# Kernel optimization log

Hardware: AMD Instinct MI355X
Metric: run time of the kernel (lower is better)

Reference implementation:

```python
import jax, jax.numpy as jnp
import numpy as np

K = 10
EPS = 1e-5  # BatchNorm eps, eval mode with running_mean=0, running_var=1


def mish(x):
    return x * jnp.tanh(jax.nn.softplus(x))


def knn_idx(x, k):
    # x: (B, C, N); returns (B, N, k) indices of k nearest neighbors (incl. self)
    xx = jnp.sum(x * x, axis=1)                      # (B, N)
    inner = jnp.einsum('bcn,bcm->bnm', x, x)         # (B, N, N)
    neg_d = 2.0 * inner - xx[:, :, None] - xx[:, None, :]
    return jax.lax.top_k(neg_d, k)[1]


def graph_feature(x, k):
    # x: (B, C, N) -> edge features (B, 2C, N, k): cat(nbr - x, x)
    idx = knn_idx(x, k)
    x_t = jnp.transpose(x, (0, 2, 1))                # (B, N, C)
    nbr = jax.vmap(lambda xt, ix: xt[ix])(x_t, idx)  # (B, N, k, C)
    ctr = jnp.broadcast_to(x_t[:, :, None, :], nbr.shape)
    edge = jnp.concatenate([nbr - ctr, ctr], axis=-1)
    return jnp.transpose(edge, (0, 3, 1, 2))


def block2d(x, W, g, b):
    # Conv2d(kernel=1, bias=False) + BatchNorm2d(eval) + Mish
    y = jnp.einsum('oi,bink->bonk', W, x)
    y = y * (g / jnp.sqrt(1.0 + EPS))[None, :, None, None] + b[None, :, None, None]
    return mish(y)


def block1d(x, W, g, b):
    # Conv1d(kernel=1, bias=False) + BatchNorm1d(eval) + Mish
    y = jnp.einsum('oi,bin->bon', W, x)
    y = y * (g / jnp.sqrt(1.0 + EPS))[None, :, None] + b[None, :, None]
    return mish(y)


def setup_inputs() -> dict:
    key = jax.random.key(0)
    ks = jax.random.split(key, 32)
    B, N = 8, 4096
    x = jax.random.normal(ks[0], (B, 3, N), dtype=jnp.float32)

    def w(k, o, i):
        return jax.random.normal(k, (o, i), dtype=jnp.float32) * np.float32(np.sqrt(2.0 / i))

    W1 = w(ks[1], 64, 6)
    W2 = w(ks[2], 64, 128)
    W3 = w(ks[3], 128, 128)
    W4 = w(ks[4], 128, 128)
    W5 = w(ks[5], 128, 256)
    W6 = w(ks[6], 64, 128)
    W7 = w(ks[7], 64, 128)
    W8 = w(ks[8], 64, 128)
    W9 = w(ks[9], 2, 64)

    bn_sizes = [64, 64, 128, 128, 128, 64, 64, 64]
    gs, bs = [], []
    for i, c in enumerate(bn_sizes):
        gs.append(1.0 + 0.1 * jax.random.normal(ks[10 + i], (c,), dtype=jnp.float32))
        bs.append(0.1 * jax.random.normal(ks[20 + i], (c,), dtype=jnp.float32))

    d = {'x': x, 'W1': W1, 'W2': W2, 'W3': W3, 'W4': W4, 'W5': W5,
         'W6': W6, 'W7': W7, 'W8': W8, 'W9': W9}
    for i in range(8):
        d['g%d' % (i + 1)] = gs[i]
        d['b%d' % (i + 1)] = bs[i]
    return d


def reference(x, W1, W2, W3, W4, W5, W6, W7, W8, W9,
              g1, g2, g3, g4, g5, g6, g7, g8,
              b1, b2, b3, b4, b5, b6, b7, b8):
    e = graph_feature(x, K)                      # (B, 6, N, k)
    x1 = jnp.max(block2d(e, W1, g1, b1), axis=-1)  # (B, 64, N)
    e = graph_feature(x1, K)                     # (B, 128, N, k)
    x2 = jnp.max(block2d(e, W2, g2, b2), axis=-1)  # (B, 64, N)
    e = graph_feature(x2, K)                     # (B, 128, N, k)
    x3 = jnp.max(block2d(e, W3, g3, b3), axis=-1)  # (B, 128, N)
    h = block1d(x3, W4, g4, b4)                  # (B, 128, N)
    h = block1d(jnp.concatenate([h, x3], axis=1), W5, g5, b5)  # (B, 128, N)
    h = block1d(h, W6, g6, b6)                   # (B, 64, N)
    h = block1d(jnp.concatenate([h, x2], axis=1), W7, g7, b7)  # (B, 64, N)
    h = block1d(jnp.concatenate([h, x1], axis=1), W8, g8, b8)  # (B, 64, N)
    return jnp.einsum('oi,bin->bon', W9, h)      # (B, 2, N)
```

## Files before the change

kernel.cpp:

```cpp
#include <hip/hip_runtime.h>
#include <hip/hip_bf16.h>
#include <math.h>
#include <float.h>

#define B_ 8
#define N_ 4096
#define M_ (B_*N_)
#define KNN 10

typedef unsigned long long ull;
typedef __attribute__((ext_vector_type(8))) short s16x8;
typedef __attribute__((ext_vector_type(4))) float f32x4;

__device__ __forceinline__ float mishf(float x){
  float sp = (x > 20.f) ? x : __logf(1.f + __expf(x));
  float e2 = __expf(-2.f*sp);
  float th = (1.f - e2) / (1.f + e2);
  return x * th;
}

__device__ __forceinline__ ull shfl_xor_u64(ull v, int mask){
  unsigned lo = (unsigned)v, hi = (unsigned)(v >> 32);
  lo = (unsigned)__shfl_xor((int)lo, mask);
  hi = (unsigned)__shfl_xor((int)hi, mask);
  return ((ull)hi << 32) | lo;
}
__device__ __forceinline__ ull shfl_u64(ull v, int src){
  unsigned lo = (unsigned)v, hi = (unsigned)(v >> 32);
  lo = (unsigned)__shfl((int)lo, src);
  hi = (unsigned)__shfl((int)hi, src);
  return ((ull)hi << 32) | lo;
}
__device__ __forceinline__ int mbcnt_lt(ull mask){
  return __builtin_amdgcn_mbcnt_hi((unsigned)(mask>>32),
         __builtin_amdgcn_mbcnt_lo((unsigned)mask, 0));
}
__device__ __forceinline__ unsigned mono_u32(float f){
  unsigned u = __float_as_uint(f);
  return u ^ ((unsigned)((int)u >> 31) | 0x80000000u);
}
__device__ __forceinline__ float unmono(unsigned vk){
  unsigned u = (vk & 0x80000000u) ? (vk ^ 0x80000000u) : ~vk;
  return __uint_as_float(u);
}

__global__ __launch_bounds__(256) void k_transpose_x(const float* __restrict__ x,
                                                     float* __restrict__ xp){
  int n = blockIdx.x*256 + threadIdx.x;
  if (n >= M_) return;
  int b = n >> 12, i = n & (N_-1);
  const float* xb = x + (size_t)b*3*N_;
  float v0 = xb[i], v1 = xb[N_+i], v2 = xb[2*N_+i];
  float* o = xp + (size_t)n*3;
  o[0]=v0; o[1]=v1; o[2]=v2;
}

template<int C>
__global__ __launch_bounds__(256) void k_xx(const float* __restrict__ X,
                                            float* __restrict__ xx){
  int n = blockIdx.x*256 + threadIdx.x;
  if (n >= M_) return;
  const float* r = X + (size_t)n*C;
  float s = 0.f;
#pragma unroll
  for (int c=0;c<C;c++){ float v=r[c]; s = fmaf(v,v,s); }
  xx[n] = s;
}

__global__ __launch_bounds__(256) void k_cvt(const float* __restrict__ X,
                                             ushort* __restrict__ Xhi,
                                             ushort* __restrict__ Xlo){
  int i = blockIdx.x*256 + threadIdx.x;
  const float4* src = (const float4*)X + (size_t)i*2;
  float4 v0 = src[0], v1 = src[1];
  float vv[8] = {v0.x,v0.y,v0.z,v0.w,v1.x,v1.y,v1.z,v1.w};
  ushort h[8], l[8];
#pragma unroll
  for (int e=0;e<8;e++){
    __hip_bfloat16 hb = __float2bfloat16(vv[e]);
    float hf = __bfloat162float(hb);
    __hip_bfloat16 lb = __float2bfloat16(vv[e]-hf);
    h[e] = *(ushort*)&hb; l[e] = *(ushort*)&lb;
  }
  uint4 hp, lp;
  hp.x = (unsigned)h[0] | ((unsigned)h[1]<<16);
  hp.y = (unsigned)h[2] | ((unsigned)h[3]<<16);
  hp.z = (unsigned)h[4] | ((unsigned)h[5]<<16);
  hp.w = (unsigned)h[6] | ((unsigned)h[7]<<16);
  lp.x = (unsigned)l[0] | ((unsigned)l[1]<<16);
  lp.y = (unsigned)l[2] | ((unsigned)l[3]<<16);
  lp.z = (unsigned)l[4] | ((unsigned)l[5]<<16);
  lp.w = (unsigned)l[6] | ((unsigned)l[7]<<16);
  *(uint4*)(Xhi + (size_t)i*8) = hp;
  *(uint4*)(Xlo + (size_t)i*8) = lp;
}

__global__ __launch_bounds__(256,2) void k_knn64m(const ushort* __restrict__ Xhi,
                                                  const ushort* __restrict__ Xlo,
                                                  const float* __restrict__ xx,
                                                  int* __restrict__ idxout){
  constexpr int JT  = 128;
  constexpr int CAP = 320;
  __shared__ ushort XJhi[JT*64];
  __shared__ ushort XJlo[JT*64];
  __shared__ float  halfxx[JT];
  __shared__ ull    buf[4][CAP];

  const int t    = threadIdx.x;
  const int w    = t >> 6;
  const int lane = t & 63;
  const int b    = blockIdx.x & 7;
  const int i0   = (blockIdx.x >> 3) * 64;
  const float* xxb = xx + (size_t)b*N_;

  const int arow = i0 + w*16 + (lane & 15);
  const ushort* Ah = Xhi + ((size_t)(b*N_ + arow))*64;
  const ushort* Al = Xlo + ((size_t)(b*N_ + arow))*64;
  const int ko = (lane >> 4)*8;
  s16x8 aH0 = *(const s16x8*)(Ah + ko);
  s16x8 aH1 = *(const s16x8*)(Ah + 32 + ko);
  s16x8 aL0 = *(const s16x8*)(Al + ko);
  s16x8 aL1 = *(const s16x8*)(Al + 32 + ko);

  ull kq[KNN];
#pragma unroll
  for (int q=0;q<KNN;q++) kq[q]=0ull;
  float Treg = -INFINITY;

  for (int jt = 0; jt < N_/JT; ++jt){
    const int j0 = jt*JT;
    {
      const int r = t & 127;
      const ushort* src = ((t < 128) ? Xhi : Xlo) + ((size_t)(b*N_ + j0 + r))*64;
      char* dst = (char*)((t < 128) ? XJhi : XJlo) + r*128;
      const unsigned sw = ((unsigned)(r & 7)) << 4;
#pragma unroll
      for (int c=0;c<8;c++){
        uint4 v = *(const uint4*)(src + c*8);
        *(uint4*)(dst + ((unsigned)(c*16) ^ sw)) = v;
      }
    }
    if (t < JT) halfxx[t] = 0.5f*xxb[j0+t];
    __syncthreads();

    f32x4 acc[8];
#pragma unroll
    for (int cb=0;cb<8;cb++) acc[cb] = (f32x4){0.f,0.f,0.f,0.f};

#pragma unroll
    for (int cb=0;cb<8;cb++){
      const int brow = cb*16 + (lane & 15);
      const unsigned sw = ((unsigned)(brow & 7)) << 4;
      const char* ph = (const char*)XJhi + brow*128;
      const char* pl = (const char*)XJlo + brow*128;
      const int kb0 = (int)((unsigned)((lane>>4)<<4) ^ sw);
      const int kb1 = (int)((unsigned)(64 | ((lane>>4)<<4)) ^ sw);
      s16x8 bh0 = *(const s16x8*)(ph + kb0);
      s16x8 bl0 = *(const s16x8*)(pl + kb0);
      s16x8 bh1 = *(const s16x8*)(ph + kb1);
      s16x8 bl1 = *(const s16x8*)(pl + kb1);
      f32x4 a = acc[cb];
      a = __builtin_amdgcn_mfma_f32_16x16x32_bf16(aH0, bh0, a, 0,0,0);
      a = __builtin_amdgcn_mfma_f32_16x16x32_bf16(aH0, bl0, a, 0,0,0);
      a = __builtin_amdgcn_mfma_f32_16x16x32_bf16(aL0, bh0, a, 0,0,0);
      a = __builtin_amdgcn_mfma_f32_16x16x32_bf16(aL0, bl0, a, 0,0,0);
      a = __builtin_amdgcn_mfma_f32_16x16x32_bf16(aH1, bh1, a, 0,0,0);
      a = __builtin_amdgcn_mfma_f32_16x16x32_bf16(aH1, bl1, a, 0,0,0);
      a = __builtin_amdgcn_mfma_f32_16x16x32_bf16(aL1, bh1, a, 0,0,0);
      a = __builtin_amdgcn_mfma_f32_16x16x32_bf16(aL1, bl1, a, 0,0,0);
      acc[cb] = a;
    }

    float hx[8];
#pragma unroll
    for (int cb=0;cb<8;cb++) hx[cb] = halfxx[cb*16 + (lane & 15)];

    if (jt == 0){
#pragma unroll
      for (int reg=0;reg<4;reg++){
        const unsigned rl = (unsigned)((lane>>4)*4 + reg);
        ull k8[8];
#pragma unroll
        for (int cb=0;cb<8;cb++){
          float v = acc[cb][reg] - hx[cb];
          unsigned jinv = 4095u - (unsigned)(cb*16 + (lane & 15));
          k8[cb] = ((ull)mono_u32(v)<<32) | ((ull)jinv<<4) | rl;
        }
#pragma unroll
        for (int q=0;q<KNN;q++){
          ull m = k8[0];
#pragma unroll
          for (int s=1;s<8;s++) m = m > k8[s] ? m : k8[s];
          ull v1 = shfl_xor_u64(m,1); m = m>v1?m:v1;
          ull v2 = shfl_xor_u64(m,2); m = m>v2?m:v2;
          ull v4 = shfl_xor_u64(m,4); m = m>v4?m:v4;
          ull v8 = shfl_xor_u64(m,8); m = m>v8?m:v8;
          ull mv = shfl_u64(m, (lane>>2)<<4);
          if (lane < 16 && (lane&3)==reg) kq[q] = mv;
#pragma unroll
          for (int s=0;s<8;s++) k8[s] = (k8[s]==m) ? 0ull : k8[s];
        }
      }
      Treg = unmono((unsigned)(kq[KNN-1] >> 32));
    } else {
      float Tf[4];
#pragma unroll
      for (int reg=0;reg<4;reg++) Tf[reg] = __shfl(Treg, (lane>>4)*4 + reg);
      int cnt = 0;
#pragma unroll
      for (int cb=0;cb<8;cb++){
#pragma unroll
        for (int reg=0;reg<4;reg++){
          float v = acc[cb][reg] - hx[cb];
          bool pass = v >= Tf[reg];
          ull mask = __ballot(pass);
          if (mask){
            if (pass){
              int slot = cnt + mbcnt_lt(mask);
              unsigned jinv = 4095u - (unsigned)(j0 + cb*16 + (lane & 15));
              ull key = ((ull)mono_u32(v)<<32) | ((ull)jinv<<4)
                        | (unsigned)((lane>>4)*4 + reg);
              if (slot < CAP) buf[w][slot] = key;
            }
            cnt += __popcll(mask);
          }
        }
      }
      if (cnt){
        int nb = cnt < CAP ? cnt : CAP;
        for (int e=0;e<nb;e++){
          ull k64 = buf[w][e];
          if ((int)(k64 & 15ull) == lane && k64 > kq[KNN-1]){
            ull ck = k64;
#pragma unroll
            for (int q=0;q<KNN;q++){
              ull hi = ck > kq[q] ? ck : kq[q];
              ull lo = ck > kq[q] ? kq[q] : ck;
              kq[q] = hi; ck = lo;
            }
          }
        }
        Treg = unmono((unsigned)(kq[KNN-1] >> 32));
      }
    }
    __syncthreads();
  }

  if (lane < 16){
    int* o = idxout + ((size_t)b*N_ + i0 + w*16 + lane)*KNN;
#pragma unroll
    for (int q=0;q<KNN;q++) o[q] = (int)(4095u - (unsigned)((kq[q]>>4) & 4095ull));
  }
}

template<int C>
__global__ __launch_bounds__(256,2) void k_knn(const float* __restrict__ X,
                                               const float* __restrict__ xx,
                                               int* __restrict__ idxout){
  constexpr bool BIG = (C % 4 == 0);
  constexpr int LS  = BIG ? (C + 4) : 12;
  constexpr int NC4 = BIG ? (C/4 + 1) : 1;
  constexpr int JT  = 128;
  constexpr int CAP = 320;
  __shared__ float XI[64*LS];
  __shared__ float XJ[JT*LS];
  __shared__ ull   buf[4][CAP];

  const int t    = threadIdx.x;
  const int w    = t >> 6;
  const int lane = t & 63;
  const int b    = blockIdx.y;
  const int i0   = blockIdx.x*64;
  const int tc   = t & 15, tr = t >> 4;
  const float* Xb  = X  + (size_t)b*N_*C;
  const float* xxb = xx + (size_t)b*N_;

  if constexpr (BIG){
    for (int f = t; f < 64*(C/4); f += 256){
      int r = f >> 4, c4 = f & 15;
      *(float4*)&XI[r*LS + c4*4] = *(const float4*)&Xb[(size_t)(i0+r)*C + c4*4];
    }
    if (t < 64){ XI[t*LS+C]=1.f; XI[t*LS+C+1]=0.f; XI[t*LS+C+2]=0.f; XI[t*LS+C+3]=0.f; }
  } else {
    if (t < 64){
      const float* p = &Xb[(size_t)(i0+t)*C];
      XI[t*LS+0]=p[0]; XI[t*LS+1]=p[1]; XI[t*LS+2]=p[2]; XI[t*LS+3]=1.f;
    }
  }

  ull kq[KNN];
#pragma unroll
  for (int q=0;q<KNN;q++) kq[q]=0ull;
  float Treg = -INFINITY;

  for (int jt = 0; jt < N_/JT; ++jt){
    const int j0 = jt*JT;
    if constexpr (BIG){
      for (int f = t; f < JT*(C/4); f += 256){
        int r = f >> 4, c4 = f & 15;
        *(float4*)&XJ[r*LS + c4*4] = *(const float4*)&Xb[(size_t)(j0+r)*C + c4*4];
      }
      if (t < JT){ XJ[t*LS+C] = -0.5f*xxb[j0+t]; XJ[t*LS+C+1]=0.f; XJ[t*LS+C+2]=0.f; XJ[t*LS+C+3]=0.f; }
    } else {
      if (t < JT){
        const float* p = &Xb[(size_t)(j0+t)*C];
        XJ[t*LS+0]=p[0]; XJ[t*LS+1]=p[1]; XJ[t*LS+2]=p[2]; XJ[t*LS+3]=-0.5f*xxb[j0+t];
      }
    }
    __syncthreads();

    float acc[4][8];
#pragma unroll
    for (int rr=0;rr<4;rr++)
#pragma unroll
      for (int s=0;s<8;s++) acc[rr][s]=0.f;

#pragma unroll 2
    for (int c4 = 0; c4 < NC4; ++c4){
      float4 xi0 = *(const float4*)&XI[(tr*4+0)*LS + c4*4];
      float4 xi1 = *(const float4*)&XI[(tr*4+1)*LS + c4*4];
      float4 xi2 = *(const float4*)&XI[(tr*4+2)*LS + c4*4];
      float4 xi3 = *(const float4*)&XI[(tr*4+3)*LS + c4*4];
#pragma unroll
      for (int s=0;s<8;s++){
        float4 xj = *(const float4*)&XJ[(tc+16*s)*LS + c4*4];
        float a0=acc[0][s], a1=acc[1][s], a2=acc[2][s], a3=acc[3][s];
        a0=fmaf(xi0.x,xj.x,a0); a1=fmaf(xi1.x,xj.x,a1); a2=fmaf(xi2.x,xj.x,a2); a3=fmaf(xi3.x,xj.x,a3);
        a0=fmaf(xi0.y,xj.y,a0); a1=fmaf(xi1.y,xj.y,a1); a2=fmaf(xi2.y,xj.y,a2); a3=fmaf(xi3.y,xj.y,a3);
        a0=fmaf(xi0.z,xj.z,a0); a1=fmaf(xi1.z,xj.z,a1); a2=fmaf(xi2.z,xj.z,a2); a3=fmaf(xi3.z,xj.z,a3);
        a0=fmaf(xi0.w,xj.w,a0); a1=fmaf(xi1.w,xj.w,a1); a2=fmaf(xi2.w,xj.w,a2); a3=fmaf(xi3.w,xj.w,a3);
        acc[0][s]=a0; acc[1][s]=a1; acc[2][s]=a2; acc[3][s]=a3;
      }
    }

    if (jt == 0){
#pragma unroll
      for (int rr=0;rr<4;rr++){
        const unsigned rl = (unsigned)((lane>>4)*4 + rr);
        ull k8[8];
#pragma unroll
        for (int s=0;s<8;s++){
          unsigned jinv = 4095u - (unsigned)(tc + 16*s);
          k8[s] = ((ull)mono_u32(acc[rr][s])<<32) | ((ull)jinv<<4) | rl;
        }
#pragma unroll
        for (int q=0;q<KNN;q++){
          ull m = k8[0];
#pragma unroll
          for (int s=1;s<8;s++) m = m > k8[s] ? m : k8[s];
          ull v1 = shfl_xor_u64(m,1); m = m>v1?m:v1;
          ull v2 = shfl_xor_u64(m,2); m = m>v2?m:v2;
          ull v4 = shfl_xor_u64(m,4); m = m>v4?m:v4;
          ull v8 = shfl_xor_u64(m,8); m = m>v8?m:v8;
          ull mv = shfl_u64(m, (lane>>2)<<4);
          if (lane < 16 && (lane&3)==rr) kq[q] = mv;
#pragma unroll
          for (int s=0;s<8;s++) k8[s] = (k8[s]==m) ? 0ull : k8[s];
        }
      }
      Treg = unmono((unsigned)(kq[KNN-1] >> 32));
    } else {
      float Tf[4];
#pragma unroll
      for (int rr=0;rr<4;rr++) Tf[rr] = __shfl(Treg, (lane>>4)*4 + rr);
      int cnt = 0;
#pragma unroll
      for (int s=0;s<8;s++){
#pragma unroll
        for (int rr=0;rr<4;rr++){
          bool pass = acc[rr][s] >= Tf[rr];
          ull mask = __ballot(pass);
          if (mask){
            if (pass){
              int slot = cnt + mbcnt_lt(mask);
              unsigned jinv = 4095u - (unsigned)(j0 + tc + 16*s);
              ull key = ((ull)mono_u32(acc[rr][s])<<32) | ((ull)jinv<<4)
                        | (unsigned)((lane>>4)*4 + rr);
              if (slot < CAP) buf[w][slot] = key;
            }
            cnt += __popcll(mask);
          }
        }
      }
      if (cnt){
        int nb = cnt < CAP ? cnt : CAP;
        for (int e=0;e<nb;e++){
          ull k64 = buf[w][e];
          if ((int)(k64 & 15ull) == lane && k64 > kq[KNN-1]){
            ull ck = k64;
#pragma unroll
            for (int q=0;q<KNN;q++){
              ull hi = ck > kq[q] ? ck : kq[q];
              ull lo = ck > kq[q] ? kq[q] : ck;
              kq[q] = hi; ck = lo;
            }
          }
        }
        Treg = unmono((unsigned)(kq[KNN-1] >> 32));
      }
    }
    __syncthreads();
  }

  if (lane < 16){
    int* o = idxout + ((size_t)b*N_ + i0 + w*16 + lane)*KNN;
#pragma unroll
    for (int q=0;q<KNN;q++) o[q] = (int)(4095u - (unsigned)((kq[q]>>4) & 4095ull));
  }
}

template<int PT>
__global__ __launch_bounds__(256) void k_gemm(
    const float* __restrict__ X1, int C1,
    const float* __restrict__ X2, int C2,
    const float* __restrict__ W, int hmask, int hshift, int wstride, int hoff,
    const float* __restrict__ g, const float* __restrict__ bb, int act,
    float* __restrict__ Y, int Pfull)
{
  constexpr int CPT = PT/16;
  constexpr int WLS = PT + 4;
  __shared__ float Xt[32*68];
  __shared__ float Wt[32*WLS];
  const int t  = threadIdx.x;
  const int r0 = blockIdx.x*64;
  const int p0 = blockIdx.y*PT;
  const int cg = t & 15, rg = t >> 4;
  const int C = C1 + C2;
  const int nkt = (C + 31) >> 5;

  float acc[4][CPT];
#pragma unroll
  for (int a=0;a<4;a++)
#pragma unroll
    for (int c=0;c<CPT;c++) acc[a][c]=0.f;

  for (int kt = 0; kt < nkt; ++kt){
    const int k0 = kt*32;
#pragma unroll
    for (int e = t; e < 64*32; e += 256){
      int kk = e & 31, r = e >> 5;
      int gk = k0 + kk;
      float v = 0.f;
      if (gk < C1) v = X1[(size_t)(r0+r)*C1 + gk];
      else if (gk < C) v = X2[(size_t)(r0+r)*C2 + (gk - C1)];
      Xt[kk*68 + r] = v;
    }
#pragma unroll
    for (int e = t; e < PT*32; e += 256){
      int kk = e & 31, p = e >> 5;
      int gp = p0 + p;
      int wrow = (gp & hmask)*wstride + (gp >> hshift)*hoff;
      int gk = k0 + kk;
      Wt[kk*WLS + p] = (gk < C) ? W[(size_t)wrow + gk] : 0.f;
    }
    __syncthreads();
#pragma unroll
    for (int kk=0;kk<32;kk++){
      float4 xv = *(const float4*)&Xt[kk*68 + rg*4];
      float xr[4] = {xv.x, xv.y, xv.z, xv.w};
      float wv[CPT];
#pragma unroll
      for (int c4=0;c4<CPT/4;c4++){
        float4 w4 = *(const float4*)&Wt[kk*WLS + cg*CPT + c4*4];
        wv[c4*4+0]=w4.x; wv[c4*4+1]=w4.y; wv[c4*4+2]=w4.z; wv[c4*4+3]=w4.w;
      }
#pragma unroll
      for (int rr=0;rr<4;rr++)
#pragma unroll
        for (int cc=0;cc<CPT;cc++)
          acc[rr][cc] = fmaf(xr[rr], wv[cc], acc[rr][cc]);
    }
    __syncthreads();
  }

  const float srs = rsqrtf(1.f + 1e-5f);
  float sv[CPT], bvv[CPT];
#pragma unroll
  for (int cc=0;cc<CPT;cc++){
    int gp = p0 + cg*CPT + cc;
    if (g){ sv[cc] = g[gp]*srs; bvv[cc] = bb[gp]; } else { sv[cc]=1.f; bvv[cc]=0.f; }
  }
#pragma unroll
  for (int rr=0;rr<4;rr++){
    size_t row = r0 + rg*4 + rr;
    float* yr = Y + row*(size_t)Pfull + p0 + cg*CPT;
#pragma unroll
    for (int c4=0;c4<CPT/4;c4++){
      float y0 = sv[c4*4+0]*acc[rr][c4*4+0] + bvv[c4*4+0];
      float y1 = sv[c4*4+1]*acc[rr][c4*4+1] + bvv[c4*4+1];
      float y2 = sv[c4*4+2]*acc[rr][c4*4+2] + bvv[c4*4+2];
      float y3 = sv[c4*4+3]*acc[rr][c4*4+3] + bvv[c4*4+3];
      if (act){ y0=mishf(y0); y1=mishf(y1); y2=mishf(y2); y3=mishf(y3); }
      *(float4*)&yr[c4*4] = make_float4(y0,y1,y2,y3);
    }
  }
}

template<int O>
__global__ __launch_bounds__(256) void k_edgemax(
    const float* __restrict__ ua, const int* __restrict__ idx,
    const float* __restrict__ g, const float* __restrict__ bb,
    float* __restrict__ Y)
{
  constexpr int TPR = O/4;
  const int gt = blockIdx.x*256 + threadIdx.x;
  const int m  = gt / TPR;
  const int og = gt % TPR;
  if (m >= M_) return;
  const int base = m & ~(N_-1);
  const int P = 2*O;
  const float4 u0 = *(const float4*)&ua[(size_t)m*P + og*4];
  const float4 a0 = *(const float4*)&ua[(size_t)m*P + O + og*4];
  const float srs = rsqrtf(1.f + 1e-5f);
  const float4 gv  = *(const float4*)&g[og*4];
  const float4 bv4 = *(const float4*)&bb[og*4];
  const float sx = gv.x*srs, sy = gv.y*srs, sz = gv.z*srs, sw = gv.w*srs;
  const float cx = a0.x - u0.x, cy = a0.y - u0.y, cz = a0.z - u0.z, cw = a0.w - u0.w;
  float mx = -INFINITY, my = -INFINITY, mz = -INFINITY, mw = -INFINITY;
  const int* id = idx + (size_t)m*KNN;
#pragma unroll
  for (int k=0;k<KNN;k++){
    int j = id[k];
    const float4 uj = *(const float4*)&ua[(size_t)(base + j)*P + og*4];
    float zx = fmaf(sx, uj.x + cx, bv4.x);
    float zy = fmaf(sy, uj.y + cy, bv4.y);
    float zz = fmaf(sz, uj.z + cz, bv4.z);
    float zw = fmaf(sw, uj.w + cw, bv4.w);
    mx = fmaxf(mx, mishf(zx));
    my = fmaxf(my, mishf(zy));
    mz = fmaxf(mz, mishf(zz));
    mw = fmaxf(mw, mishf(zw));
  }
  *(float4*)&Y[(size_t)m*O + og*4] = make_float4(mx,my,mz,mw);
}

__global__ __launch_bounds__(256) void k_final(const float* __restrict__ h,
                                               const float* __restrict__ W9,
                                               float* __restrict__ out){
  __shared__ float w[128];
  const int t = threadIdx.x;
  if (t < 128) w[t] = W9[t];
  __syncthreads();
  const int m = blockIdx.x*256 + t;
  if (m >= M_) return;
  const int b = m >> 12, i = m & (N_-1);
  const float* hr = h + (size_t)m*64;
  float s0 = 0.f, s1 = 0.f;
#pragma unroll
  for (int c=0;c<64;c++){ float v = hr[c]; s0 = fmaf(w[c], v, s0); s1 = fmaf(w[64+c], v, s1); }
  out[((size_t)b*2 + 0)*N_ + i] = s0;
  out[((size_t)b*2 + 1)*N_ + i] = s1;
}

extern "C" void kernel_launch(void* const* d_in, const int* in_sizes, int n_in,
                              void* d_out, int out_size, void* d_ws, size_t ws_size,
                              hipStream_t stream)
{
  const float* x  = (const float*)d_in[0];
  const float* W1 = (const float*)d_in[1];
  const float* W2 = (const float*)d_in[2];
  const float* W3 = (const float*)d_in[3];
  const float* W4 = (const float*)d_in[4];
  const float* W5 = (const float*)d_in[5];
  const float* W6 = (const float*)d_in[6];
  const float* W7 = (const float*)d_in[7];
  const float* W8 = (const float*)d_in[8];
  const float* W9 = (const float*)d_in[9];
  const float* g1 = (const float*)d_in[10]; const float* b1 = (const float*)d_in[11];
  const float* g2 = (const float*)d_in[12]; const float* b2 = (const float*)d_in[13];
  const float* g3 = (const float*)d_in[14]; const float* b3 = (const float*)d_in[15];
  const float* g4 = (const float*)d_in[16]; const float* b4 = (const float*)d_in[17];
  const float* g5 = (const float*)d_in[18]; const float* b5 = (const float*)d_in[19];
  const float* g6 = (const float*)d_in[20]; const float* b6 = (const float*)d_in[21];
  const float* g7 = (const float*)d_in[22]; const float* b7 = (const float*)d_in[23];
  const float* g8 = (const float*)d_in[24]; const float* b8 = (const float*)d_in[25];
  float* out = (float*)d_out;

  float* ws  = (float*)d_ws;
  float* xp  = ws;
  float* xx  = xp + 98304;
  int*   idx = (int*)(xx + 32768);
  float* ua  = (float*)(idx + 327680);
  float* x1  = ua + 8388608;
  float* x2  = x1 + 2097152;
  float* x3  = x2 + 2097152;
  float* h4  = x3 + 4194304;
  float* h5  = h4 + 4194304;
  float* h6  = x3;
  float* h7  = h4;
  float* h8  = h5;
  ushort* Xhi = (ushort*)ua;
  ushort* Xlo = (ushort*)(ua + 1048576);

  const dim3 blk(256);
  const float* nullf = nullptr;

  k_transpose_x<<<dim3(M_/256), blk, 0, stream>>>(x, xp);
  k_xx<3><<<dim3(M_/256), blk, 0, stream>>>(xp, xx);
  k_knn<3><<<dim3(N_/64, B_), blk, 0, stream>>>(xp, xx, idx);
  k_gemm<128><<<dim3(M_/64, 1), blk, 0, stream>>>(xp, 3, nullf, 0,
      W1, 63, 6, 6, 3, nullf, nullf, 0, ua, 128);
  k_edgemax<64><<<dim3(M_*16/256), blk, 0, stream>>>(ua, idx, g1, b1, x1);

  k_xx<64><<<dim3(M_/256), blk, 0, stream>>>(x1, xx);
  k_cvt<<<dim3(M_*64/(8*256)), blk, 0, stream>>>(x1, Xhi, Xlo);
  k_knn64m<<<dim3(512), blk, 0, stream>>>(Xhi, Xlo, xx, idx);
  k_gemm<128><<<dim3(M_/64, 1), blk, 0, stream>>>(x1, 64, nullf, 0,
      W2, 63, 6, 128, 64, nullf, nullf, 0, ua, 128);
  k_edgemax<64><<<dim3(M_*16/256), blk, 0, stream>>>(ua, idx, g2, b2, x2);

  k_xx<64><<<dim3(M_/256), blk, 0, stream>>>(x2, xx);
  k_cvt<<<dim3(M_*64/(8*256)), blk, 0, stream>>>(x2, Xhi, Xlo);
  k_knn64m<<<dim3(512), blk, 0, stream>>>(Xhi, Xlo, xx, idx);
  k_gemm<128><<<dim3(M_/64, 2), blk, 0, stream>>>(x2, 64, nullf, 0,
      W3, 127, 7, 128, 64, nullf, nullf, 0, ua, 256);
  k_edgemax<128><<<dim3(M_*32/256), blk, 0, stream>>>(ua, idx, g3, b3, x3);

  k_gemm<128><<<dim3(M_/64, 1), blk, 0, stream>>>(x3, 128, nullf, 0,
      W4, 127, 7, 128, 0, g4, b4, 1, h4, 128);
  k_gemm<128><<<dim3(M_/64, 1), blk, 0, stream>>>(h4, 128, x3, 128,
      W5, 127, 7, 256, 0, g5, b5, 1, h5, 128);
  k_gemm<64><<<dim3(M_/64, 1), blk, 0, stream>>>(h5, 128, nullf, 0,
      W6, 63, 6, 128, 0, g6, b6, 1, h6, 64);
  k_gemm<64><<<dim3(M_/64, 1), blk, 0, stream>>>(h6, 64, x2, 64,
      W7, 63, 6, 128, 0, g7, b7, 1, h7, 64);
  k_gemm<64><<<dim3(M_/64, 1), blk, 0, stream>>>(h7, 64, x1, 64,
      W8, 63, 6, 128, 0, g8, b8, 1, h8, 64);
  k_final<<<dim3(M_/256), blk, 0, stream>>>(h8, W9, out);
}
```

Baseline: 1.647 ms.

## Split KNN candidate range in halves across blocks and merge partial top-k

```diff
diff --git a/kernel.cpp b/kernel.cpp
--- a/kernel.cpp
+++ b/kernel.cpp
@@ -95,11 +95,11 @@
   *(uint4*)(Xlo + (size_t)i*8) = lp;
 }
 
-__global__ __launch_bounds__(256,2) void k_knn64m(const ushort* __restrict__ Xhi,
+__global__ __launch_bounds__(256,4) void k_knn64m(const ushort* __restrict__ Xhi,
                                                   const ushort* __restrict__ Xlo,
                                                   const float* __restrict__ xx,
-                                                  int* __restrict__ idxout){
-  constexpr int JT  = 128;
+                                                  ull* __restrict__ part){
+  constexpr int JT  = 64;
   constexpr int CAP = 320;
   __shared__ ushort XJhi[JT*64];
   __shared__ ushort XJlo[JT*64];
@@ -109,8 +109,12 @@
   const int t    = threadIdx.x;
   const int w    = t >> 6;
   const int lane = t & 63;
-  const int b    = blockIdx.x & 7;
-  const int i0   = (blockIdx.x >> 3) * 64;
+  const int bid  = blockIdx.x;
+  const int b    = bid & 7;
+  const int rest = bid >> 3;
+  const int i0   = (rest >> 1) * 64;
+  const int half = rest & 1;
+  const int jbase = half * 2048;
   const float* xxb = xx + (size_t)b*N_;
 
   const int arow = i0 + w*16 + (lane & 15);
@@ -127,28 +131,30 @@
   for (int q=0;q<KNN;q++) kq[q]=0ull;
   float Treg = -INFINITY;
 
-  for (int jt = 0; jt < N_/JT; ++jt){
-    const int j0 = jt*JT;
+  for (int jt = 0; jt < 2048/JT; ++jt){
+    const int j0g = jbase + jt*JT;
     {
-      const int r = t & 127;
-      const ushort* src = ((t < 128) ? Xhi : Xlo) + ((size_t)(b*N_ + j0 + r))*64;
-      char* dst = (char*)((t < 128) ? XJhi : XJlo) + r*128;
+      const int bsel = t >> 7;
+      const int r    = (t >> 1) & 63;
+      const int cq   = (t & 1) * 4;
+      const ushort* src = (bsel ? Xlo : Xhi) + ((size_t)(b*N_ + j0g + r))*64 + cq*8;
+      char* dst = (char*)(bsel ? XJlo : XJhi) + r*128;
       const unsigned sw = ((unsigned)(r & 7)) << 4;
 #pragma unroll
-      for (int c=0;c<8;c++){
+      for (int c=0;c<4;c++){
         uint4 v = *(const uint4*)(src + c*8);
-        *(uint4*)(dst + ((unsigned)(c*16) ^ sw)) = v;
-      }
-    }
-    if (t < JT) halfxx[t] = 0.5f*xxb[j0+t];
+        *(uint4*)(dst + ((unsigned)((cq+c)*16) ^ sw)) = v;
+      }
+    }
+    if (t < JT) halfxx[t] = 0.5f*xxb[j0g+t];
     __syncthreads();
 
-    f32x4 acc[8];
-#pragma unroll
-    for (int cb=0;cb<8;cb++) acc[cb] = (f32x4){0.f,0.f,0.f,0.f};
-
-#pragma unroll
-    for (int cb=0;cb<8;cb++){
+    f32x4 acc[4];
+#pragma unroll
+    for (int cb=0;cb<4;cb++) acc[cb] = (f32x4){0.f,0.f,0.f,0.f};
+
+#pragma unroll
+    for (int cb=0;cb<4;cb++){
       const int brow = cb*16 + (lane & 15);
       const unsigned sw = ((unsigned)(brow & 7)) << 4;
       const char* ph = (const char*)XJhi + brow*128;
@@ -171,26 +177,26 @@
       acc[cb] = a;
     }
 
-    float hx[8];
-#pragma unroll
-    for (int cb=0;cb<8;cb++) hx[cb] = halfxx[cb*16 + (lane & 15)];
+    float hx[4];
+#pragma unroll
+    for (int cb=0;cb<4;cb++) hx[cb] = halfxx[cb*16 + (lane & 15)];
 
     if (jt == 0){
 #pragma unroll
       for (int reg=0;reg<4;reg++){
         const unsigned rl = (unsigned)((lane>>4)*4 + reg);
-        ull k8[8];
-#pragma unroll
-        for (int cb=0;cb<8;cb++){
+        ull k4[4];
+#pragma unroll
+        for (int cb=0;cb<4;cb++){
           float v = acc[cb][reg] - hx[cb];
-          unsigned jinv = 4095u - (unsigned)(cb*16 + (lane & 15));
-          k8[cb] = ((ull)mono_u32(v)<<32) | ((ull)jinv<<4) | rl;
+          unsigned jinv = 4095u - (unsigned)(j0g + cb*16 + (lane & 15));
+          k4[cb] = ((ull)mono_u32(v)<<32) | ((ull)jinv<<4) | rl;
         }
 #pragma unroll
         for (int q=0;q<KNN;q++){
-          ull m = k8[0];
-#pragma unroll
-          for (int s=1;s<8;s++) m = m > k8[s] ? m : k8[s];
+          ull m = k4[0];
+#pragma unroll
+          for (int s=1;s<4;s++) m = m > k4[s] ? m : k4[s];
           ull v1 = shfl_xor_u64(m,1); m = m>v1?m:v1;
           ull v2 = shfl_xor_u64(m,2); m = m>v2?m:v2;
           ull v4 = shfl_xor_u64(m,4); m = m>v4?m:v4;
@@ -198,7 +204,7 @@
           ull mv = shfl_u64(m, (lane>>2)<<4);
           if (lane < 16 && (lane&3)==reg) kq[q] = mv;
 #pragma unroll
-          for (int s=0;s<8;s++) k8[s] = (k8[s]==m) ? 0ull : k8[s];
+          for (int s=0;s<4;s++) k4[s] = (k4[s]==m) ? 0ull : k4[s];
         }
       }
       Treg = unmono((unsigned)(kq[KNN-1] >> 32));
@@ -208,7 +214,7 @@
       for (int reg=0;reg<4;reg++) Tf[reg] = __shfl(Treg, (lane>>4)*4 + reg);
       int cnt = 0;
 #pragma unroll
-      for (int cb=0;cb<8;cb++){
+      for (int cb=0;cb<4;cb++){
 #pragma unroll
         for (int reg=0;reg<4;reg++){
           float v = acc[cb][reg] - hx[cb];
@@ -217,7 +223,7 @@
           if (mask){
             if (pass){
               int slot = cnt + mbcnt_lt(mask);
-              unsigned jinv = 4095u - (unsigned)(j0 + cb*16 + (lane & 15));
+              unsigned jinv = 4095u - (unsigned)(j0g + cb*16 + (lane & 15));
               ull key = ((ull)mono_u32(v)<<32) | ((ull)jinv<<4)
                         | (unsigned)((lane>>4)*4 + reg);
               if (slot < CAP) buf[w][slot] = key;
@@ -228,15 +234,22 @@
       }
       if (cnt){
         int nb = cnt < CAP ? cnt : CAP;
-        for (int e=0;e<nb;e++){
-          ull k64 = buf[w][e];
-          if ((int)(k64 & 15ull) == lane && k64 > kq[KNN-1]){
-            ull ck = k64;
-#pragma unroll
-            for (int q=0;q<KNN;q++){
-              ull hi = ck > kq[q] ? ck : kq[q];
-              ull lo = ck > kq[q] ? kq[q] : ck;
-              kq[q] = hi; ck = lo;
+        int pad = (4 - (nb & 3)) & 3;
+        if (lane < pad && nb + lane < CAP) buf[w][nb + lane] = 0ull;
+        int nb4 = nb + pad; if (nb4 > CAP) nb4 = CAP;
+        for (int e=0;e<nb4;e+=4){
+          ull c0=buf[w][e+0], c1=buf[w][e+1], c2=buf[w][e+2], c3=buf[w][e+3];
+#pragma unroll
+          for (int u=0;u<4;u++){
+            ull k64 = (u==0)?c0:(u==1)?c1:(u==2)?c2:c3;
+            if ((int)(k64 & 15ull) == lane && k64 > kq[KNN-1]){
+              ull ck = k64;
+#pragma unroll
+              for (int q=0;q<KNN;q++){
+                ull hi = ck > kq[q] ? ck : kq[q];
+                ull lo = ck > kq[q] ? kq[q] : ck;
+                kq[q] = hi; ck = lo;
+              }
             }
           }
         }
@@ -247,16 +260,16 @@
   }
 
   if (lane < 16){
-    int* o = idxout + ((size_t)b*N_ + i0 + w*16 + lane)*KNN;
-#pragma unroll
-    for (int q=0;q<KNN;q++) o[q] = (int)(4095u - (unsigned)((kq[q]>>4) & 4095ull));
+    ull* o = part + ((size_t)((b*N_ + i0 + w*16 + lane)*2 + half))*KNN;
+#pragma unroll
+    for (int q=0;q<KNN;q++) o[q] = kq[q];
   }
 }
 
 template<int C>
-__global__ __launch_bounds__(256,2) void k_knn(const float* __restrict__ X,
+__global__ __launch_bounds__(256,4) void k_knn(const float* __restrict__ X,
                                                const float* __restrict__ xx,
-                                               int* __restrict__ idxout){
+                                               ull* __restrict__ part){
   constexpr bool BIG = (C % 4 == 0);
   constexpr int LS  = BIG ? (C + 4) : 12;
   constexpr int NC4 = BIG ? (C/4 + 1) : 1;
@@ -269,8 +282,12 @@
   const int t    = threadIdx.x;
   const int w    = t >> 6;
   const int lane = t & 63;
-  const int b    = blockIdx.y;
-  const int i0   = blockIdx.x*64;
+  const int bid  = blockIdx.x;
+  const int b    = bid & 7;
+  const int rest = bid >> 3;
+  const int i0   = (rest >> 1) * 64;
+  const int half = rest & 1;
+  const int jbase = half * 2048;
   const int tc   = t & 15, tr = t >> 4;
   const float* Xb  = X  + (size_t)b*N_*C;
   const float* xxb = xx + (size_t)b*N_;
@@ -293,8 +310,8 @@
   for (int q=0;q<KNN;q++) kq[q]=0ull;
   float Treg = -INFINITY;
 
-  for (int jt = 0; jt < N_/JT; ++jt){
-    const int j0 = jt*JT;
+  for (int jt = 0; jt < 2048/JT; ++jt){
+    const int j0 = jbase + jt*JT;
     if constexpr (BIG){
       for (int f = t; f < JT*(C/4); f += 256){
         int r = f >> 4, c4 = f & 15;
@@ -340,7 +357,7 @@
         ull k8[8];
 #pragma unroll
         for (int s=0;s<8;s++){
-          unsigned jinv = 4095u - (unsigned)(tc + 16*s);
+          unsigned jinv = 4095u - (unsigned)(j0 + tc + 16*s);
           k8[s] = ((ull)mono_u32(acc[rr][s])<<32) | ((ull)jinv<<4) | rl;
         }
 #pragma unroll
@@ -384,15 +401,22 @@
       }
       if (cnt){
         int nb = cnt < CAP ? cnt : CAP;
-        for (int e=0;e<nb;e++){
-          ull k64 = buf[w][e];
-          if ((int)(k64 & 15ull) == lane && k64 > kq[KNN-1]){
-            ull ck = k64;
-#pragma unroll
-            for (int q=0;q<KNN;q++){
-              ull hi = ck > kq[q] ? ck : kq[q];
-              ull lo = ck > kq[q] ? kq[q] : ck;
-              kq[q] = hi; ck = lo;
+        int pad = (4 - (nb & 3)) & 3;
+        if (lane < pad && nb + lane < CAP) buf[w][nb + lane] = 0ull;
+        int nb4 = nb + pad; if (nb4 > CAP) nb4 = CAP;
+        for (int e=0;e<nb4;e+=4){
+          ull c0=buf[w][e+0], c1=buf[w][e+1], c2=buf[w][e+2], c3=buf[w][e+3];
+#pragma unroll
+          for (int u=0;u<4;u++){
+            ull k64 = (u==0)?c0:(u==1)?c1:(u==2)?c2:c3;
+            if ((int)(k64 & 15ull) == lane && k64 > kq[KNN-1]){
+              ull ck = k64;
+#pragma unroll
+              for (int q=0;q<KNN;q++){
+                ull hi = ck > kq[q] ? ck : kq[q];
+                ull lo = ck > kq[q] ? kq[q] : ck;
+                kq[q] = hi; ck = lo;
+              }
             }
           }
         }
@@ -403,9 +427,28 @@
   }
 
   if (lane < 16){
-    int* o = idxout + ((size_t)b*N_ + i0 + w*16 + lane)*KNN;
-#pragma unroll
-    for (int q=0;q<KNN;q++) o[q] = (int)(4095u - (unsigned)((kq[q]>>4) & 4095ull));
+    ull* o = part + ((size_t)((b*N_ + i0 + w*16 + lane)*2 + half))*KNN;
+#pragma unroll
+    for (int q=0;q<KNN;q++) o[q] = kq[q];
+  }
+}
+
+__global__ __launch_bounds__(256) void k_knnmerge(const ull* __restrict__ part,
+                                                  int* __restrict__ idxout){
+  int row = blockIdx.x*256 + threadIdx.x;
+  if (row >= M_) return;
+  const ull* pa = part + (size_t)row*2*KNN;
+  const ull* pb = pa + KNN;
+  int ia=0, ib=0;
+  int* o = idxout + (size_t)row*KNN;
+#pragma unroll
+  for (int s=0;s<KNN;s++){
+    ull ka = (ia < KNN) ? pa[ia] : 0ull;
+    ull kb = (ib < KNN) ? pb[ib] : 0ull;
+    bool ta = ka > kb;
+    ull k = ta ? ka : kb;
+    o[s] = (int)(4095u - (unsigned)((k>>4) & 4095ull));
+    ia += ta ? 1 : 0; ib += ta ? 0 : 1;
   }
 }
 
@@ -591,27 +634,31 @@
   float* h8  = h5;
   ushort* Xhi = (ushort*)ua;
   ushort* Xlo = (ushort*)(ua + 1048576);
+  ull*    part = (ull*)(ua + 2097152);
 
   const dim3 blk(256);
   const float* nullf = nullptr;
 
   k_transpose_x<<<dim3(M_/256), blk, 0, stream>>>(x, xp);
   k_xx<3><<<dim3(M_/256), blk, 0, stream>>>(xp, xx);
-  k_knn<3><<<dim3(N_/64, B_), blk, 0, stream>>>(xp, xx, idx);
+  k_knn<3><<<dim3(1024), blk, 0, stream>>>(xp, xx, part);
+  k_knnmerge<<<dim3(M_/256), blk, 0, stream>>>(part, idx);
   k_gemm<128><<<dim3(M_/64, 1), blk, 0, stream>>>(xp, 3, nullf, 0,
       W1, 63, 6, 6, 3, nullf, nullf, 0, ua, 128);
   k_edgemax<64><<<dim3(M_*16/256), blk, 0, stream>>>(ua, idx, g1, b1, x1);
 
   k_xx<64><<<dim3(M_/256), blk, 0, stream>>>(x1, xx);
   k_cvt<<<dim3(M_*64/(8*256)), blk, 0, stream>>>(x1, Xhi, Xlo);
-  k_knn64m<<<dim3(512), blk, 0, stream>>>(Xhi, Xlo, xx, idx);
+  k_knn64m<<<dim3(1024), blk, 0, stream>>>(Xhi, Xlo, xx, part);
+  k_knnmerge<<<dim3(M_/256), blk, 0, stream>>>(part, idx);
   k_gemm<128><<<dim3(M_/64, 1), blk, 0, stream>>>(x1, 64, nullf, 0,
       W2, 63, 6, 128, 64, nullf, nullf, 0, ua, 128);
   k_edgemax<64><<<dim3(M_*16/256), blk, 0, stream>>>(ua, idx, g2, b2, x2);
 
   k_xx<64><<<dim3(M_/256), blk, 0, stream>>>(x2, xx);
   k_cvt<<<dim3(M_*64/(8*256)), blk, 0, stream>>>(x2, Xhi, Xlo);
-  k_knn64m<<<dim3(512), blk, 0, stream>>>(Xhi, Xlo, xx, idx);
+  k_knn64m<<<dim3(1024), blk, 0, stream>>>(Xhi, Xlo, xx, part);
+  k_knnmerge<<<dim3(M_/256), blk, 0, stream>>>(part, idx);
   k_gemm<128><<<dim3(M_/64, 2), blk, 0, stream>>>(x2, 64, nullf, 0,
       W3, 127, 7, 128, 64, nullf, nullf, 0, ua, 256);
   k_edgemax<128><<<dim3(M_*32/256), blk, 0, stream>>>(ua, idx, g3, b3, x3);
```

Result: slower. 1.941 ms (+17.9%).

## Double-buffer KNN j-tiles in LDS with register prefetch; unroll candidate scan

Applied to the files above, without the earlier changes.

```diff
diff --git a/kernel.cpp b/kernel.cpp
--- a/kernel.cpp
+++ b/kernel.cpp
@@ -101,9 +101,9 @@
                                                   int* __restrict__ idxout){
   constexpr int JT  = 128;
   constexpr int CAP = 320;
-  __shared__ ushort XJhi[JT*64];
-  __shared__ ushort XJlo[JT*64];
-  __shared__ float  halfxx[JT];
+  __shared__ ushort XJhi[2][JT*64];
+  __shared__ ushort XJlo[2][JT*64];
+  __shared__ float  halfxx[2][JT];
   __shared__ ull    buf[4][CAP];
 
   const int t    = threadIdx.x;
@@ -127,21 +127,33 @@
   for (int q=0;q<KNN;q++) kq[q]=0ull;
   float Treg = -INFINITY;
 
+  const int sr = t & 127;
+  const ushort* sbase = ((t < 128) ? Xhi : Xlo) + ((size_t)(b*N_))*64;
+  const unsigned ssw = ((unsigned)(sr & 7)) << 4;
+
+  uint4 stg[8]; float hstg = 0.f;
+  {
+    const ushort* src = sbase + ((size_t)sr)*64;
+#pragma unroll
+    for (int c=0;c<8;c++) stg[c] = *(const uint4*)(src + c*8);
+    if (t < JT) hstg = 0.5f*xxb[t];
+    char* dst = (char*)((t < 128) ? XJhi[0] : XJlo[0]) + sr*128;
+#pragma unroll
+    for (int c=0;c<8;c++) *(uint4*)(dst + ((unsigned)(c*16) ^ ssw)) = stg[c];
+    if (t < JT) halfxx[0][t] = hstg;
+  }
+  __syncthreads();
+
   for (int jt = 0; jt < N_/JT; ++jt){
+    const int cur = jt & 1;
     const int j0 = jt*JT;
-    {
-      const int r = t & 127;
-      const ushort* src = ((t < 128) ? Xhi : Xlo) + ((size_t)(b*N_ + j0 + r))*64;
-      char* dst = (char*)((t < 128) ? XJhi : XJlo) + r*128;
-      const unsigned sw = ((unsigned)(r & 7)) << 4;
-#pragma unroll
-      for (int c=0;c<8;c++){
-        uint4 v = *(const uint4*)(src + c*8);
-        *(uint4*)(dst + ((unsigned)(c*16) ^ sw)) = v;
-      }
-    }
-    if (t < JT) halfxx[t] = 0.5f*xxb[j0+t];
-    __syncthreads();
+
+    if (jt < N_/JT - 1){
+      const ushort* src = sbase + ((size_t)(j0 + JT + sr))*64;
+#pragma unroll
+      for (int c=0;c<8;c++) stg[c] = *(const uint4*)(src + c*8);
+      if (t < JT) hstg = 0.5f*xxb[j0 + JT + t];
+    }
 
     f32x4 acc[8];
 #pragma unroll
@@ -151,8 +163,8 @@
     for (int cb=0;cb<8;cb++){
       const int brow = cb*16 + (lane & 15);
       const unsigned sw = ((unsigned)(brow & 7)) << 4;
-      const char* ph = (const char*)XJhi + brow*128;
-      const char* pl = (const char*)XJlo + brow*128;
+      const char* ph = (const char*)XJhi[cur] + brow*128;
+      const char* pl = (const char*)XJlo[cur] + brow*128;
       const int kb0 = (int)((unsigned)((lane>>4)<<4) ^ sw);
       const int kb1 = (int)((unsigned)(64 | ((lane>>4)<<4)) ^ sw);
       s16x8 bh0 = *(const s16x8*)(ph + kb0);
@@ -173,7 +185,14 @@
 
     float hx[8];
 #pragma unroll
-    for (int cb=0;cb<8;cb++) hx[cb] = halfxx[cb*16 + (lane & 15)];
+    for (int cb=0;cb<8;cb++) hx[cb] = halfxx[cur][cb*16 + (lane & 15)];
+
+    if (jt < N_/JT - 1){
+      char* dst = (char*)((t < 128) ? XJhi[cur^1] : XJlo[cur^1]) + sr*128;
+#pragma unroll
+      for (int c=0;c<8;c++) *(uint4*)(dst + ((unsigned)(c*16) ^ ssw)) = stg[c];
+      if (t < JT) halfxx[cur^1][t] = hstg;
+    }
 
     if (jt == 0){
 #pragma unroll
@@ -228,15 +247,22 @@
       }
       if (cnt){
         int nb = cnt < CAP ? cnt : CAP;
-        for (int e=0;e<nb;e++){
-          ull k64 = buf[w][e];
-          if ((int)(k64 & 15ull) == lane && k64 > kq[KNN-1]){
-            ull ck = k64;
-#pragma unroll
-            for (int q=0;q<KNN;q++){
-              ull hi = ck > kq[q] ? ck : kq[q];
-              ull lo = ck > kq[q] ? kq[q] : ck;
-              kq[q] = hi; ck = lo;
+        int pad = (4 - (nb & 3)) & 3;
+        if (lane < pad && nb + lane < CAP) buf[w][nb + lane] = 0ull;
+        int nb4 = nb + pad; if (nb4 > CAP) nb4 = CAP;
+        for (int e=0;e<nb4;e+=4){
+          ull c0=buf[w][e+0], c1=buf[w][e+1], c2=buf[w][e+2], c3=buf[w][e+3];
+#pragma unroll
+          for (int u=0;u<4;u++){
+            ull k64 = (u==0)?c0:(u==1)?c1:(u==2)?c2:c3;
+            if ((int)(k64 & 15ull) == lane && k64 > kq[KNN-1]){
+              ull ck = k64;
+#pragma unroll
+              for (int q=0;q<KNN;q++){
+                ull hi = ck > kq[q] ? ck : kq[q];
+                ull lo = ck > kq[q] ? kq[q] : ck;
+                kq[q] = hi; ck = lo;
+              }
             }
           }
         }
```

Measured after the change: 1.617 ms. Within noise of the previous version (-1.8%).
